# Optimization experiments

Measured on AMD Instinct MI355X. Metric: run time of the kernel, lower is better.

Reference implementation:

```python
import jax, jax.numpy as jnp
import numpy as np

B, A, C, H, S, NR = 128, 2048, 128, 512, 3, 2
PR = C + 3 + S   # 134 read params per head
PW = 3 * C + 3 + S  # 390 write params


def setup_inputs() -> dict:
    key = jax.random.key(0)
    ks = jax.random.split(key, 8)
    h = jax.random.normal(ks[0], (B, H), jnp.float32)
    mem = jax.random.normal(ks[1], (B, A, C), jnp.float32)
    ra = jax.random.uniform(ks[2], (NR, B, A), jnp.float32)
    ra = ra / ra.sum(-1, keepdims=True)  # valid attention distributions
    wa = jax.random.uniform(ks[3], (B, A), jnp.float32)
    wa = wa / wa.sum(-1, keepdims=True)
    W_read = 0.02 * jax.random.normal(ks[4], (NR, PR, H), jnp.float32)
    b_read = jnp.zeros((NR, PR), jnp.float32)
    W_write = 0.02 * jax.random.normal(ks[5], (PW, H), jnp.float32)
    b_write = jnp.zeros((PW,), jnp.float32)
    return dict(h=h, mem=mem, prev_read_attn=ra, prev_write_attn=wa,
                W_read=W_read, b_read=b_read, W_write=W_write, b_write=b_write)


def _addressing(query, beta, gate, shift, gamma, mem, prev_w):
    """NTM addressing. query [...,C] (raw), beta/gate/gamma [...,1], shift [...,S],
    mem [B,A,C] (broadcasts), prev_w [...,A]. Returns attention [...,A]."""
    eps = 1e-8
    q = jax.nn.sigmoid(query)
    beta = jax.nn.softplus(beta) + 1.0
    gate = jax.nn.sigmoid(gate)
    shift_w = jax.nn.softmax(shift, axis=-1)
    gamma = jax.nn.softplus(gamma) + 1.0
    # content-based addressing: cosine similarity + sharpened softmax over A
    qn = jnp.maximum(jnp.linalg.norm(q, axis=-1, keepdims=True), eps)      # [...,1]
    mn = jnp.maximum(jnp.linalg.norm(mem, axis=-1), eps)                   # [B,A]
    sim = jnp.einsum('...c,...ac->...a', q, mem) / (qn * mn)
    w_c = jax.nn.softmax(beta * sim, axis=-1)
    # gated interpolation with previous attention
    w_g = gate * w_c + (1.0 - gate) * prev_w
    # circular shift convolution, offsets -(S//2)..S//2
    K = S // 2
    idx = (jnp.arange(A)[:, None] - (jnp.arange(S)[None, :] - K)) % A      # [A,S]
    w_s = jnp.einsum('...as,...s->...a', w_g[..., idx], shift_w)
    # gamma sharpening
    w_pow = w_s ** gamma
    return w_pow / (w_pow.sum(-1, keepdims=True) + 1e-12)


def reference(h, mem, prev_read_attn, prev_write_attn, W_read, b_read, W_write, b_write):
    # --- read heads (vectorized over NR heads) ---
    pr = jnp.einsum('bh,rph->rbp', h, W_read) + b_read[:, None, :]         # [NR,B,PR]
    q, beta, gate, shift, gamma = jnp.split(pr, [C, C + 1, C + 2, C + 2 + S], axis=-1)
    read_w = _addressing(q, beta, gate, shift, gamma, mem, prev_read_attn)  # [NR,B,A]
    read_vectors = jnp.einsum('rba,bac->rbc', read_w, mem)                 # [NR,B,C]
    # --- write head ---
    pw = h @ W_write.T + b_write                                           # [B,PW]
    locs = np.cumsum([C, 1, 1, S, 1, C])
    qw, bw, gw, sw, gmw, erase, add = jnp.split(pw, locs.tolist(), axis=-1)
    write_w = _addressing(qw, bw, gw, sw, gmw, mem, prev_write_attn)       # [B,A]
    e = jax.nn.sigmoid(erase)[:, None, :]                                  # [B,1,C]
    a = jax.nn.sigmoid(add)[:, None, :]                                    # [B,1,C]
    w = write_w[..., None]                                                 # [B,A,1]
    new_mem = mem * (1.0 - w * e) + w * a
    return read_vectors, new_mem
```

## Files before the change

kernel.cpp:

```cpp
#include <hip/hip_runtime.h>
#include <math.h>

constexpr int B_  = 128;
constexpr int A_  = 2048;
constexpr int C_  = 128;
constexpr int H_  = 512;
constexpr int S_  = 3;
constexpr int NR_ = 2;
constexpr int PR_ = C_ + 3 + S_;
constexpr int PW_ = 3 * C_ + 3 + S_;

typedef float vfloat4 __attribute__((ext_vector_type(4)));

__device__ __forceinline__ float sigmoidf_(float x) { return 1.0f / (1.0f + expf(-x)); }
__device__ __forceinline__ float softplusf_(float x) {
  return fmaxf(x, 0.0f) + log1pf(expf(-fabsf(x)));
}

__device__ __forceinline__ float waveReduceSum(float v) {
#pragma unroll
  for (int off = 32; off; off >>= 1) v += __shfl_xor(v, off, 64);
  return v;
}
__device__ __forceinline__ float waveReduceMax(float v) {
#pragma unroll
  for (int off = 32; off; off >>= 1) v = fmaxf(v, __shfl_xor(v, off, 64));
  return v;
}

__global__ __launch_bounds__(256) void proj_kernel(
    const float* __restrict__ h, const float* __restrict__ Wr,
    const float* __restrict__ br, const float* __restrict__ Ww,
    const float* __restrict__ bw, float* __restrict__ pr, float* __restrict__ pw,
    float* __restrict__ rv) {
  constexpr int NPR = NR_ * B_ * PR_;
  constexpr int NPW = B_ * PW_;
  int gid = blockIdx.x * 256 + threadIdx.x;
  if (gid < NR_ * B_ * C_) rv[gid] = 0.0f;
  int wave = gid >> 6;
  int lane = threadIdx.x & 63;
  int out0 = wave * 2;
  const float* w0row;
  const float* w1row;
  const float* hrow;
  float bias0, bias1;
  float* outp;
  if (out0 < NPR) {
    int r = out0 / (B_ * PR_);
    int rem = out0 - r * (B_ * PR_);
    int b = rem / PR_;
    int p = rem - b * PR_;
    w0row = Wr + (size_t)(r * PR_ + p) * H_;
    w1row = w0row + H_;
    hrow = h + (size_t)b * H_;
    bias0 = br[r * PR_ + p];
    bias1 = br[r * PR_ + p + 1];
    outp = pr + out0;
  } else {
    int w2 = out0 - NPR;
    if (w2 >= NPW) return;
    int b = w2 / PW_;
    int p = w2 - b * PW_;
    w0row = Ww + (size_t)p * H_;
    w1row = w0row + H_;
    hrow = h + (size_t)b * H_;
    bias0 = bw[p];
    bias1 = bw[p + 1];
    outp = pw + w2;
  }
  const float4* h4 = (const float4*)hrow;
  const float4* wa4 = (const float4*)w0row;
  const float4* wb4 = (const float4*)w1row;
  float4 a0 = h4[(lane << 1)];
  float4 a1 = h4[(lane << 1) + 1];
  float4 b0 = wa4[(lane << 1)];
  float4 b1 = wa4[(lane << 1) + 1];
  float4 c0 = wb4[(lane << 1)];
  float4 c1 = wb4[(lane << 1) + 1];
  float acc0 = a0.x * b0.x;
  acc0 = fmaf(a0.y, b0.y, acc0);
  acc0 = fmaf(a0.z, b0.z, acc0);
  acc0 = fmaf(a0.w, b0.w, acc0);
  acc0 = fmaf(a1.x, b1.x, acc0);
  acc0 = fmaf(a1.y, b1.y, acc0);
  acc0 = fmaf(a1.z, b1.z, acc0);
  acc0 = fmaf(a1.w, b1.w, acc0);
  float acc1 = a0.x * c0.x;
  acc1 = fmaf(a0.y, c0.y, acc1);
  acc1 = fmaf(a0.z, c0.z, acc1);
  acc1 = fmaf(a0.w, c0.w, acc1);
  acc1 = fmaf(a1.x, c1.x, acc1);
  acc1 = fmaf(a1.y, c1.y, acc1);
  acc1 = fmaf(a1.z, c1.z, acc1);
  acc1 = fmaf(a1.w, c1.w, acc1);
  acc0 = waveReduceSum(acc0);
  acc1 = waveReduceSum(acc1);
  if (lane == 0) {
    outp[0] = acc0 + bias0;
    outp[1] = acc1 + bias1;
  }
}

__global__ __launch_bounds__(256) void sim_kernel(
    const float* __restrict__ mem, const float* __restrict__ pr,
    const float* __restrict__ pw, float* __restrict__ sim) {
  __shared__ __align__(16) float qs[3 * C_];
  __shared__ float iqn[3];
  int b = blockIdx.x >> 5;
  int chunk = blockIdx.x & 31;
  int rowbase = chunk << 6;
  int tid = threadIdx.x;
  for (int idx = tid; idx < 3 * C_; idx += 256) {
    int hd = idx >> 7;
    int c = idx & (C_ - 1);
    float raw = (hd < 2) ? pr[(size_t)(hd * B_ + b) * PR_ + c]
                         : pw[(size_t)b * PW_ + c];
    qs[idx] = sigmoidf_(raw);
  }
  __syncthreads();
  int wv = tid >> 6;
  int lane = tid & 63;
  if (wv < 3) {
    float v0 = qs[wv * C_ + lane];
    float v1 = qs[wv * C_ + 64 + lane];
    float ss = v0 * v0 + v1 * v1;
    ss = waveReduceSum(ss);
    if (lane == 0) iqn[wv] = 1.0f / fmaxf(sqrtf(ss), 1e-8f);
  }
  __syncthreads();

  int j = lane & 7;
  int rsub = lane >> 3;

  float4 q0[4], q1[4], q2[4];
  const float4* qs4 = (const float4*)qs;
#pragma unroll
  for (int k = 0; k < 4; k++) {
    q0[k] = qs4[j + 8 * k];
    q1[k] = qs4[32 + j + 8 * k];
    q2[k] = qs4[64 + j + 8 * k];
  }
  float iqn0 = iqn[0], iqn1 = iqn[1], iqn2 = iqn[2];

#pragma unroll
  for (int it = 0; it < 2; it++) {
    int row = rowbase + (it << 5) + (wv << 3) + rsub;
    const float4* mrow = (const float4*)(mem + ((size_t)b * A_ + row) * C_);
    float d0 = 0.f, d1 = 0.f, d2 = 0.f, ss = 0.f;
#pragma unroll
    for (int k = 0; k < 4; k++) {
      float4 m = mrow[j + 8 * k];
      d0 = fmaf(m.x, q0[k].x, d0); d0 = fmaf(m.y, q0[k].y, d0);
      d0 = fmaf(m.z, q0[k].z, d0); d0 = fmaf(m.w, q0[k].w, d0);
      d1 = fmaf(m.x, q1[k].x, d1); d1 = fmaf(m.y, q1[k].y, d1);
      d1 = fmaf(m.z, q1[k].z, d1); d1 = fmaf(m.w, q1[k].w, d1);
      d2 = fmaf(m.x, q2[k].x, d2); d2 = fmaf(m.y, q2[k].y, d2);
      d2 = fmaf(m.z, q2[k].z, d2); d2 = fmaf(m.w, q2[k].w, d2);
      ss = fmaf(m.x, m.x, ss); ss = fmaf(m.y, m.y, ss);
      ss = fmaf(m.z, m.z, ss); ss = fmaf(m.w, m.w, ss);
    }
#pragma unroll
    for (int off = 1; off <= 4; off <<= 1) {
      d0 += __shfl_xor(d0, off, 64);
      d1 += __shfl_xor(d1, off, 64);
      d2 += __shfl_xor(d2, off, 64);
      ss += __shfl_xor(ss, off, 64);
    }
    if (j == 0) {
      float imn = 1.0f / fmaxf(sqrtf(ss), 1e-8f);
      sim[(size_t)(0 * B_ + b) * A_ + row] = d0 * iqn0 * imn;
      sim[(size_t)(1 * B_ + b) * A_ + row] = d1 * iqn1 * imn;
      sim[(size_t)(2 * B_ + b) * A_ + row] = d2 * iqn2 * imn;
    }
  }
}

__global__ __launch_bounds__(1024) void attn_kernel(
    const float* __restrict__ sim, const float* __restrict__ ra,
    const float* __restrict__ wa, const float* __restrict__ pr,
    const float* __restrict__ pw, float* __restrict__ attn) {
  __shared__ float wg[A_];
  __shared__ float rb1[16], rb2[16], rb3[16];
  int hb = blockIdx.x;
  int hd = hb >> 7;
  int b = hb & (B_ - 1);
  int tid = threadIdx.x;
  int wv = tid >> 6;
  int lane = tid & 63;
  const float* src = (hd < 2) ? (pr + (size_t)hb * PR_) : (pw + (size_t)b * PW_);
  float braw = src[C_];
  float graw = src[C_ + 1];
  float s0r = src[C_ + 2], s1r = src[C_ + 3], s2r = src[C_ + 4];
  float gmraw = src[C_ + 5];
  float mx3 = fmaxf(s0r, fmaxf(s1r, s2r));
  float e0 = expf(s0r - mx3), e1 = expf(s1r - mx3), e2 = expf(s2r - mx3);
  float sinv = 1.0f / (e0 + e1 + e2);
  float beta = softplusf_(braw) + 1.0f;
  float gate = sigmoidf_(graw);
  float sw0 = e0 * sinv, sw1 = e1 * sinv, sw2 = e2 * sinv;
  float gamma = softplusf_(gmraw) + 1.0f;

  const float* simrow = sim + (size_t)hb * A_;
  const float* prev = (hd < 2) ? (ra + (size_t)hb * A_) : (wa + (size_t)b * A_);
  float* outrow = attn + (size_t)hb * A_;

  int a0 = tid;
  int a1 = tid + 1024;
  float s0 = simrow[a0];
  float s1 = simrow[a1];
  float pv0 = prev[a0];
  float pv1 = prev[a1];

  float mx = fmaxf(s0, s1);
  mx = waveReduceMax(mx);
  if (lane == 0) rb1[wv] = mx;
  __syncthreads();
  float M = rb1[0];
#pragma unroll
  for (int i = 1; i < 16; i++) M = fmaxf(M, rb1[i]);

  float p0 = expf(beta * (s0 - M));
  float p1 = expf(beta * (s1 - M));
  float l = p0 + p1;
  l = waveReduceSum(l);
  if (lane == 0) rb2[wv] = l;
  __syncthreads();
  float T = rb2[0];
#pragma unroll
  for (int i = 1; i < 16; i++) T += rb2[i];
  float inv = 1.0f / T;

  wg[a0] = fmaf(gate, p0 * inv, (1.0f - gate) * pv0);
  wg[a1] = fmaf(gate, p1 * inv, (1.0f - gate) * pv1);
  __syncthreads();

  float ws0 = sw0 * wg[(a0 + 1) & (A_ - 1)] + sw1 * wg[a0] + sw2 * wg[(a0 - 1) & (A_ - 1)];
  float ws1 = sw0 * wg[(a1 + 1) & (A_ - 1)] + sw1 * wg[a1] + sw2 * wg[(a1 - 1) & (A_ - 1)];
  float wp0 = (ws0 > 0.0f) ? exp2f(gamma * log2f(ws0)) : 0.0f;
  float wp1 = (ws1 > 0.0f) ? exp2f(gamma * log2f(ws1)) : 0.0f;
  float l2 = wp0 + wp1;
  l2 = waveReduceSum(l2);
  if (lane == 0) rb3[wv] = l2;
  __syncthreads();
  float T2 = rb3[0];
#pragma unroll
  for (int i = 1; i < 16; i++) T2 += rb3[i];
  float inv2 = 1.0f / (T2 + 1e-12f);

  outrow[a0] = wp0 * inv2;
  outrow[a1] = wp1 * inv2;
}

__global__ __launch_bounds__(256) void update_kernel(
    const float* __restrict__ mem, const float* __restrict__ attn,
    const float* __restrict__ pw, float* __restrict__ rv,
    float* __restrict__ nmem) {
  __shared__ float att0[256], att1[256], attw[256];
  __shared__ float4 red0[128];
  __shared__ float4 red1[128];
  int b = blockIdx.x >> 3;
  int chunk = blockIdx.x & 7;
  int rowbase = chunk << 8;
  int tid = threadIdx.x;
  att0[tid] = attn[(size_t)(0 * B_ + b) * A_ + rowbase + tid];
  att1[tid] = attn[(size_t)(1 * B_ + b) * A_ + rowbase + tid];
  attw[tid] = attn[(size_t)(2 * B_ + b) * A_ + rowbase + tid];
  __syncthreads();

  int rowlane = tid & 31;
  int rowoff = tid >> 5;
  int c0 = rowlane << 2;
  const float* pwrow = pw + (size_t)b * PW_;
  float2 eA = *(const float2*)(pwrow + C_ + 6 + c0);
  float2 eB = *(const float2*)(pwrow + C_ + 6 + c0 + 2);
  float2 aA = *(const float2*)(pwrow + 2 * C_ + 6 + c0);
  float2 aB = *(const float2*)(pwrow + 2 * C_ + 6 + c0 + 2);
  float e0 = sigmoidf_(eA.x), e1 = sigmoidf_(eA.y), e2 = sigmoidf_(eB.x), e3 = sigmoidf_(eB.y);
  float ad0 = sigmoidf_(aA.x), ad1 = sigmoidf_(aA.y), ad2 = sigmoidf_(aB.x), ad3 = sigmoidf_(aB.y);

  float4 acc0 = make_float4(0.f, 0.f, 0.f, 0.f);
  float4 acc1 = make_float4(0.f, 0.f, 0.f, 0.f);

#pragma unroll 4
  for (int i = 0; i < 32; i++) {
    int ridx = (i << 3) + rowoff;
    int row = rowbase + ridx;
    size_t base = ((size_t)b * A_ + row) * C_ + c0;
    float4 m = *(const float4*)(mem + base);
    float w0 = att0[ridx];
    float w1 = att1[ridx];
    float ww = attw[ridx];
    acc0.x = fmaf(w0, m.x, acc0.x);
    acc0.y = fmaf(w0, m.y, acc0.y);
    acc0.z = fmaf(w0, m.z, acc0.z);
    acc0.w = fmaf(w0, m.w, acc0.w);
    acc1.x = fmaf(w1, m.x, acc1.x);
    acc1.y = fmaf(w1, m.y, acc1.y);
    acc1.z = fmaf(w1, m.z, acc1.z);
    acc1.w = fmaf(w1, m.w, acc1.w);
    vfloat4 nm;
    nm.x = fmaf(m.x, 1.0f - ww * e0, ww * ad0);
    nm.y = fmaf(m.y, 1.0f - ww * e1, ww * ad1);
    nm.z = fmaf(m.z, 1.0f - ww * e2, ww * ad2);
    nm.w = fmaf(m.w, 1.0f - ww * e3, ww * ad3);
    __builtin_nontemporal_store(nm, (vfloat4*)(nmem + base));
  }

  int lane = tid & 63;
  int wv = tid >> 6;
  acc0.x += __shfl_xor(acc0.x, 32, 64);
  acc0.y += __shfl_xor(acc0.y, 32, 64);
  acc0.z += __shfl_xor(acc0.z, 32, 64);
  acc0.w += __shfl_xor(acc0.w, 32, 64);
  acc1.x += __shfl_xor(acc1.x, 32, 64);
  acc1.y += __shfl_xor(acc1.y, 32, 64);
  acc1.z += __shfl_xor(acc1.z, 32, 64);
  acc1.w += __shfl_xor(acc1.w, 32, 64);
  if (lane < 32) {
    red0[wv * 32 + lane] = acc0;
    red1[wv * 32 + lane] = acc1;
  }
  __syncthreads();
  if (tid < 32) {
    float4 r0 = red0[tid];
    float4 t;
    t = red0[tid + 32]; r0.x += t.x; r0.y += t.y; r0.z += t.z; r0.w += t.w;
    t = red0[tid + 64]; r0.x += t.x; r0.y += t.y; r0.z += t.z; r0.w += t.w;
    t = red0[tid + 96]; r0.x += t.x; r0.y += t.y; r0.z += t.z; r0.w += t.w;
    float4 r1 = red1[tid];
    t = red1[tid + 32]; r1.x += t.x; r1.y += t.y; r1.z += t.z; r1.w += t.w;
    t = red1[tid + 64]; r1.x += t.x; r1.y += t.y; r1.z += t.z; r1.w += t.w;
    t = red1[tid + 96]; r1.x += t.x; r1.y += t.y; r1.z += t.z; r1.w += t.w;
    float* rv0 = rv + (size_t)(0 * B_ + b) * C_ + (tid << 2);
    float* rv1 = rv + (size_t)(1 * B_ + b) * C_ + (tid << 2);
    atomicAdd(rv0 + 0, r0.x);
    atomicAdd(rv0 + 1, r0.y);
    atomicAdd(rv0 + 2, r0.z);
    atomicAdd(rv0 + 3, r0.w);
    atomicAdd(rv1 + 0, r1.x);
    atomicAdd(rv1 + 1, r1.y);
    atomicAdd(rv1 + 2, r1.z);
    atomicAdd(rv1 + 3, r1.w);
  }
}

extern "C" void kernel_launch(void* const* d_in, const int* in_sizes, int n_in,
                              void* d_out, int out_size, void* d_ws, size_t ws_size,
                              hipStream_t stream) {
  const float* h   = (const float*)d_in[0];
  const float* mem = (const float*)d_in[1];
  const float* ra  = (const float*)d_in[2];
  const float* wa  = (const float*)d_in[3];
  const float* Wr  = (const float*)d_in[4];
  const float* br  = (const float*)d_in[5];
  const float* Ww  = (const float*)d_in[6];
  const float* bw  = (const float*)d_in[7];

  float* out = (float*)d_out;
  float* rv = out;
  float* nmem = out + NR_ * B_ * C_;

  float* ws = (float*)d_ws;
  float* pr_buf = ws;
  float* pw_buf = pr_buf + NR_ * B_ * PR_;
  float* simb   = pw_buf + B_ * PW_;

  constexpr int NPAIRS = (NR_ * B_ * PR_ + B_ * PW_) / 2;
  proj_kernel<<<dim3(NPAIRS / 4), dim3(256), 0, stream>>>(h, Wr, br, Ww, bw, pr_buf, pw_buf, rv);
  sim_kernel<<<dim3(B_ * (A_ / 64)), dim3(256), 0, stream>>>(mem, pr_buf, pw_buf, simb);
  attn_kernel<<<dim3(3 * B_), dim3(1024), 0, stream>>>(simb, ra, wa, pr_buf, pw_buf, simb);
  update_kernel<<<dim3(B_ * (A_ / 256)), dim3(256), 0, stream>>>(mem, simb, pw_buf, rv, nmem);
}
```

Measured before the change: 289.1 us.

## Fuse similarity, addressing and memory update into one per-batch kernel

The separate sim, attention and update kernels are merged into a single kernel with one 1024-thread block per batch element. Similarities and attention weights now stay in shared memory instead of round-tripping through a workspace buffer. The read vectors are reduced in-block and stored directly, which removes the atomics and the zero-init of the output in the projection kernel. The cost is that the grid shrinks to 128 blocks, which may leave many compute units idle. Each block also streams its 1 MB memory slice twice, relying on cache for the second pass.

```diff
diff --git a/kernel.cpp b/kernel.cpp
--- a/kernel.cpp
+++ b/kernel.cpp
@@ -31,13 +31,10 @@
 __global__ __launch_bounds__(256) void proj_kernel(
     const float* __restrict__ h, const float* __restrict__ Wr,
     const float* __restrict__ br, const float* __restrict__ Ww,
-    const float* __restrict__ bw, float* __restrict__ pr, float* __restrict__ pw,
-    float* __restrict__ rv) {
+    const float* __restrict__ bw, float* __restrict__ pr, float* __restrict__ pw) {
   constexpr int NPR = NR_ * B_ * PR_;
   constexpr int NPW = B_ * PW_;
-  int gid = blockIdx.x * 256 + threadIdx.x;
-  if (gid < NR_ * B_ * C_) rv[gid] = 0.0f;
-  int wave = gid >> 6;
+  int wave = (blockIdx.x * blockDim.x + threadIdx.x) >> 6;
   int lane = threadIdx.x & 63;
   int out0 = wave * 2;
   const float* w0row;
@@ -101,25 +98,31 @@
   }
 }
 
-__global__ __launch_bounds__(256) void sim_kernel(
-    const float* __restrict__ mem, const float* __restrict__ pr,
-    const float* __restrict__ pw, float* __restrict__ sim) {
+__global__ __launch_bounds__(1024) void mega_kernel(
+    const float* __restrict__ mem, const float* __restrict__ ra,
+    const float* __restrict__ wa, const float* __restrict__ pr,
+    const float* __restrict__ pw, float* __restrict__ rv,
+    float* __restrict__ nmem) {
+  __shared__ float sims[3][A_];
+  __shared__ float wg[A_];
   __shared__ __align__(16) float qs[3 * C_];
   __shared__ float iqn[3];
-  int b = blockIdx.x >> 5;
-  int chunk = blockIdx.x & 31;
-  int rowbase = chunk << 6;
+  __shared__ float rbuf[16];
+  __shared__ float4 red[2][16][32];
+
+  int b = blockIdx.x;
   int tid = threadIdx.x;
-  for (int idx = tid; idx < 3 * C_; idx += 256) {
-    int hd = idx >> 7;
-    int c = idx & (C_ - 1);
+  int lane = tid & 63;
+  int wv = tid >> 6;
+
+  if (tid < 3 * C_) {
+    int hd = tid >> 7;
+    int c = tid & (C_ - 1);
     float raw = (hd < 2) ? pr[(size_t)(hd * B_ + b) * PR_ + c]
                          : pw[(size_t)b * PW_ + c];
-    qs[idx] = sigmoidf_(raw);
+    qs[tid] = sigmoidf_(raw);
   }
   __syncthreads();
-  int wv = tid >> 6;
-  int lane = tid & 63;
   if (wv < 3) {
     float v0 = qs[wv * C_ + lane];
     float v1 = qs[wv * C_ + 64 + lane];
@@ -129,218 +132,185 @@
   }
   __syncthreads();
 
-  int j = lane & 7;
-  int rsub = lane >> 3;
-
-  float4 q0[4], q1[4], q2[4];
-  const float4* qs4 = (const float4*)qs;
-#pragma unroll
-  for (int k = 0; k < 4; k++) {
-    q0[k] = qs4[j + 8 * k];
-    q1[k] = qs4[32 + j + 8 * k];
-    q2[k] = qs4[64 + j + 8 * k];
-  }
-  float iqn0 = iqn[0], iqn1 = iqn[1], iqn2 = iqn[2];
-
-#pragma unroll
-  for (int it = 0; it < 2; it++) {
-    int row = rowbase + (it << 5) + (wv << 3) + rsub;
-    const float4* mrow = (const float4*)(mem + ((size_t)b * A_ + row) * C_);
-    float d0 = 0.f, d1 = 0.f, d2 = 0.f, ss = 0.f;
+  {
+    int j = tid & 7;
+    int rgrp = tid >> 3;
+    float4 q0[4], q1[4], q2[4];
+    const float4* qs4 = (const float4*)qs;
 #pragma unroll
     for (int k = 0; k < 4; k++) {
-      float4 m = mrow[j + 8 * k];
-      d0 = fmaf(m.x, q0[k].x, d0); d0 = fmaf(m.y, q0[k].y, d0);
-      d0 = fmaf(m.z, q0[k].z, d0); d0 = fmaf(m.w, q0[k].w, d0);
-      d1 = fmaf(m.x, q1[k].x, d1); d1 = fmaf(m.y, q1[k].y, d1);
-      d1 = fmaf(m.z, q1[k].z, d1); d1 = fmaf(m.w, q1[k].w, d1);
-      d2 = fmaf(m.x, q2[k].x, d2); d2 = fmaf(m.y, q2[k].y, d2);
-      d2 = fmaf(m.z, q2[k].z, d2); d2 = fmaf(m.w, q2[k].w, d2);
-      ss = fmaf(m.x, m.x, ss); ss = fmaf(m.y, m.y, ss);
-      ss = fmaf(m.z, m.z, ss); ss = fmaf(m.w, m.w, ss);
-    }
-#pragma unroll
-    for (int off = 1; off <= 4; off <<= 1) {
-      d0 += __shfl_xor(d0, off, 64);
-      d1 += __shfl_xor(d1, off, 64);
-      d2 += __shfl_xor(d2, off, 64);
-      ss += __shfl_xor(ss, off, 64);
-    }
-    if (j == 0) {
-      float imn = 1.0f / fmaxf(sqrtf(ss), 1e-8f);
-      sim[(size_t)(0 * B_ + b) * A_ + row] = d0 * iqn0 * imn;
-      sim[(size_t)(1 * B_ + b) * A_ + row] = d1 * iqn1 * imn;
-      sim[(size_t)(2 * B_ + b) * A_ + row] = d2 * iqn2 * imn;
-    }
-  }
-}
-
-__global__ __launch_bounds__(1024) void attn_kernel(
-    const float* __restrict__ sim, const float* __restrict__ ra,
-    const float* __restrict__ wa, const float* __restrict__ pr,
-    const float* __restrict__ pw, float* __restrict__ attn) {
-  __shared__ float wg[A_];
-  __shared__ float rb1[16], rb2[16], rb3[16];
-  int hb = blockIdx.x;
-  int hd = hb >> 7;
-  int b = hb & (B_ - 1);
-  int tid = threadIdx.x;
-  int wv = tid >> 6;
-  int lane = tid & 63;
-  const float* src = (hd < 2) ? (pr + (size_t)hb * PR_) : (pw + (size_t)b * PW_);
-  float braw = src[C_];
-  float graw = src[C_ + 1];
-  float s0r = src[C_ + 2], s1r = src[C_ + 3], s2r = src[C_ + 4];
-  float gmraw = src[C_ + 5];
-  float mx3 = fmaxf(s0r, fmaxf(s1r, s2r));
-  float e0 = expf(s0r - mx3), e1 = expf(s1r - mx3), e2 = expf(s2r - mx3);
-  float sinv = 1.0f / (e0 + e1 + e2);
-  float beta = softplusf_(braw) + 1.0f;
-  float gate = sigmoidf_(graw);
-  float sw0 = e0 * sinv, sw1 = e1 * sinv, sw2 = e2 * sinv;
-  float gamma = softplusf_(gmraw) + 1.0f;
-
-  const float* simrow = sim + (size_t)hb * A_;
-  const float* prev = (hd < 2) ? (ra + (size_t)hb * A_) : (wa + (size_t)b * A_);
-  float* outrow = attn + (size_t)hb * A_;
-
-  int a0 = tid;
-  int a1 = tid + 1024;
-  float s0 = simrow[a0];
-  float s1 = simrow[a1];
-  float pv0 = prev[a0];
-  float pv1 = prev[a1];
-
-  float mx = fmaxf(s0, s1);
-  mx = waveReduceMax(mx);
-  if (lane == 0) rb1[wv] = mx;
+      q0[k] = qs4[j + 8 * k];
+      q1[k] = qs4[32 + j + 8 * k];
+      q2[k] = qs4[64 + j + 8 * k];
+    }
+    float iq0 = iqn[0], iq1 = iqn[1], iq2 = iqn[2];
+#pragma unroll 2
+    for (int i = 0; i < 16; i++) {
+      int row = (i << 7) + rgrp;
+      const float4* mrow = (const float4*)(mem + ((size_t)b * A_ + row) * C_);
+      float d0 = 0.f, d1 = 0.f, d2 = 0.f, ss = 0.f;
+#pragma unroll
+      for (int k = 0; k < 4; k++) {
+        float4 m = mrow[j + 8 * k];
+        d0 = fmaf(m.x, q0[k].x, d0); d0 = fmaf(m.y, q0[k].y, d0);
+        d0 = fmaf(m.z, q0[k].z, d0); d0 = fmaf(m.w, q0[k].w, d0);
+        d1 = fmaf(m.x, q1[k].x, d1); d1 = fmaf(m.y, q1[k].y, d1);
+        d1 = fmaf(m.z, q1[k].z, d1); d1 = fmaf(m.w, q1[k].w, d1);
+        d2 = fmaf(m.x, q2[k].x, d2); d2 = fmaf(m.y, q2[k].y, d2);
+        d2 = fmaf(m.z, q2[k].z, d2); d2 = fmaf(m.w, q2[k].w, d2);
+        ss = fmaf(m.x, m.x, ss); ss = fmaf(m.y, m.y, ss);
+        ss = fmaf(m.z, m.z, ss); ss = fmaf(m.w, m.w, ss);
+      }
+#pragma unroll
+      for (int off = 1; off <= 4; off <<= 1) {
+        d0 += __shfl_xor(d0, off, 64);
+        d1 += __shfl_xor(d1, off, 64);
+        d2 += __shfl_xor(d2, off, 64);
+        ss += __shfl_xor(ss, off, 64);
+      }
+      if (j == 0) {
+        float imn = 1.0f / fmaxf(sqrtf(ss), 1e-8f);
+        sims[0][row] = d0 * iq0 * imn;
+        sims[1][row] = d1 * iq1 * imn;
+        sims[2][row] = d2 * iq2 * imn;
+      }
+    }
+  }
   __syncthreads();
-  float M = rb1[0];
-#pragma unroll
-  for (int i = 1; i < 16; i++) M = fmaxf(M, rb1[i]);
-
-  float p0 = expf(beta * (s0 - M));
-  float p1 = expf(beta * (s1 - M));
-  float l = p0 + p1;
-  l = waveReduceSum(l);
-  if (lane == 0) rb2[wv] = l;
-  __syncthreads();
-  float T = rb2[0];
-#pragma unroll
-  for (int i = 1; i < 16; i++) T += rb2[i];
-  float inv = 1.0f / T;
-
-  wg[a0] = fmaf(gate, p0 * inv, (1.0f - gate) * pv0);
-  wg[a1] = fmaf(gate, p1 * inv, (1.0f - gate) * pv1);
-  __syncthreads();
-
-  float ws0 = sw0 * wg[(a0 + 1) & (A_ - 1)] + sw1 * wg[a0] + sw2 * wg[(a0 - 1) & (A_ - 1)];
-  float ws1 = sw0 * wg[(a1 + 1) & (A_ - 1)] + sw1 * wg[a1] + sw2 * wg[(a1 - 1) & (A_ - 1)];
-  float wp0 = (ws0 > 0.0f) ? exp2f(gamma * log2f(ws0)) : 0.0f;
-  float wp1 = (ws1 > 0.0f) ? exp2f(gamma * log2f(ws1)) : 0.0f;
-  float l2 = wp0 + wp1;
-  l2 = waveReduceSum(l2);
-  if (lane == 0) rb3[wv] = l2;
-  __syncthreads();
-  float T2 = rb3[0];
-#pragma unroll
-  for (int i = 1; i < 16; i++) T2 += rb3[i];
-  float inv2 = 1.0f / (T2 + 1e-12f);
-
-  outrow[a0] = wp0 * inv2;
-  outrow[a1] = wp1 * inv2;
-}
-
-__global__ __launch_bounds__(256) void update_kernel(
-    const float* __restrict__ mem, const float* __restrict__ attn,
-    const float* __restrict__ pw, float* __restrict__ rv,
-    float* __restrict__ nmem) {
-  __shared__ float att0[256], att1[256], attw[256];
-  __shared__ float4 red0[128];
-  __shared__ float4 red1[128];
-  int b = blockIdx.x >> 3;
-  int chunk = blockIdx.x & 7;
-  int rowbase = chunk << 8;
-  int tid = threadIdx.x;
-  att0[tid] = attn[(size_t)(0 * B_ + b) * A_ + rowbase + tid];
-  att1[tid] = attn[(size_t)(1 * B_ + b) * A_ + rowbase + tid];
-  attw[tid] = attn[(size_t)(2 * B_ + b) * A_ + rowbase + tid];
-  __syncthreads();
-
-  int rowlane = tid & 31;
-  int rowoff = tid >> 5;
-  int c0 = rowlane << 2;
-  const float* pwrow = pw + (size_t)b * PW_;
-  float2 eA = *(const float2*)(pwrow + C_ + 6 + c0);
-  float2 eB = *(const float2*)(pwrow + C_ + 6 + c0 + 2);
-  float2 aA = *(const float2*)(pwrow + 2 * C_ + 6 + c0);
-  float2 aB = *(const float2*)(pwrow + 2 * C_ + 6 + c0 + 2);
-  float e0 = sigmoidf_(eA.x), e1 = sigmoidf_(eA.y), e2 = sigmoidf_(eB.x), e3 = sigmoidf_(eB.y);
-  float ad0 = sigmoidf_(aA.x), ad1 = sigmoidf_(aA.y), ad2 = sigmoidf_(aB.x), ad3 = sigmoidf_(aB.y);
-
-  float4 acc0 = make_float4(0.f, 0.f, 0.f, 0.f);
-  float4 acc1 = make_float4(0.f, 0.f, 0.f, 0.f);
+
+  for (int hd = 0; hd < 3; hd++) {
+    const float* src = (hd < 2) ? (pr + (size_t)(hd * B_ + b) * PR_)
+                                : (pw + (size_t)b * PW_);
+    float braw = src[C_];
+    float graw = src[C_ + 1];
+    float s0r = src[C_ + 2], s1r = src[C_ + 3], s2r = src[C_ + 4];
+    float gmraw = src[C_ + 5];
+    float mx3 = fmaxf(s0r, fmaxf(s1r, s2r));
+    float e0 = expf(s0r - mx3), e1 = expf(s1r - mx3), e2 = expf(s2r - mx3);
+    float sinv = 1.0f / (e0 + e1 + e2);
+    float beta = softplusf_(braw) + 1.0f;
+    float gate = sigmoidf_(graw);
+    float sw0 = e0 * sinv, sw1 = e1 * sinv, sw2 = e2 * sinv;
+    float gamma = softplusf_(gmraw) + 1.0f;
+    const float* prev = (hd < 2) ? (ra + (size_t)(hd * B_ + b) * A_)
+                                 : (wa + (size_t)b * A_);
+
+    float s0 = sims[hd][tid];
+    float s1 = sims[hd][tid + 1024];
+    float pv0 = prev[tid];
+    float pv1 = prev[tid + 1024];
+
+    float mx = fmaxf(s0, s1);
+    mx = waveReduceMax(mx);
+    if (lane == 0) rbuf[wv] = mx;
+    __syncthreads();
+    float M = rbuf[0];
+#pragma unroll
+    for (int i = 1; i < 16; i++) M = fmaxf(M, rbuf[i]);
+    __syncthreads();
+
+    float p0 = expf(beta * (s0 - M));
+    float p1 = expf(beta * (s1 - M));
+    float l = p0 + p1;
+    l = waveReduceSum(l);
+    if (lane == 0) rbuf[wv] = l;
+    __syncthreads();
+    float T = rbuf[0];
+#pragma unroll
+    for (int i = 1; i < 16; i++) T += rbuf[i];
+    float inv = 1.0f / T;
+
+    wg[tid] = fmaf(gate, p0 * inv, (1.0f - gate) * pv0);
+    wg[tid + 1024] = fmaf(gate, p1 * inv, (1.0f - gate) * pv1);
+    __syncthreads();
+
+    float ws0 = sw0 * wg[(tid + 1) & (A_ - 1)] + sw1 * wg[tid] +
+                sw2 * wg[(tid - 1) & (A_ - 1)];
+    float ws1 = sw0 * wg[(tid + 1025) & (A_ - 1)] + sw1 * wg[tid + 1024] +
+                sw2 * wg[(tid + 1023) & (A_ - 1)];
+    float wp0 = (ws0 > 0.0f) ? exp2f(gamma * log2f(ws0)) : 0.0f;
+    float wp1 = (ws1 > 0.0f) ? exp2f(gamma * log2f(ws1)) : 0.0f;
+    float l2 = wp0 + wp1;
+    l2 = waveReduceSum(l2);
+    __syncthreads();
+    if (lane == 0) rbuf[wv] = l2;
+    __syncthreads();
+    float T2 = rbuf[0];
+#pragma unroll
+    for (int i = 1; i < 16; i++) T2 += rbuf[i];
+    float inv2 = 1.0f / (T2 + 1e-12f);
+    sims[hd][tid] = wp0 * inv2;
+    sims[hd][tid + 1024] = wp1 * inv2;
+    __syncthreads();
+  }
+
+  {
+    int quad = tid & 31;
+    int rgrp = tid >> 5;
+    int c0 = quad << 2;
+    const float* pwrow = pw + (size_t)b * PW_;
+    float2 eA = *(const float2*)(pwrow + C_ + 6 + c0);
+    float2 eB = *(const float2*)(pwrow + C_ + 6 + c0 + 2);
+    float2 aA = *(const float2*)(pwrow + 2 * C_ + 6 + c0);
+    float2 aB = *(const float2*)(pwrow + 2 * C_ + 6 + c0 + 2);
+    float e0 = sigmoidf_(eA.x), e1 = sigmoidf_(eA.y), e2 = sigmoidf_(eB.x), e3 = sigmoidf_(eB.y);
+    float ad0 = sigmoidf_(aA.x), ad1 = sigmoidf_(aA.y), ad2 = sigmoidf_(aB.x), ad3 = sigmoidf_(aB.y);
+
+    float4 acc0 = make_float4(0.f, 0.f, 0.f, 0.f);
+    float4 acc1 = make_float4(0.f, 0.f, 0.f, 0.f);
 
 #pragma unroll 4
-  for (int i = 0; i < 32; i++) {
-    int ridx = (i << 3) + rowoff;
-    int row = rowbase + ridx;
-    size_t base = ((size_t)b * A_ + row) * C_ + c0;
-    float4 m = *(const float4*)(mem + base);
-    float w0 = att0[ridx];
-    float w1 = att1[ridx];
-    float ww = attw[ridx];
-    acc0.x = fmaf(w0, m.x, acc0.x);
-    acc0.y = fmaf(w0, m.y, acc0.y);
-    acc0.z = fmaf(w0, m.z, acc0.z);
-    acc0.w = fmaf(w0, m.w, acc0.w);
-    acc1.x = fmaf(w1, m.x, acc1.x);
-    acc1.y = fmaf(w1, m.y, acc1.y);
-    acc1.z = fmaf(w1, m.z, acc1.z);
-    acc1.w = fmaf(w1, m.w, acc1.w);
-    vfloat4 nm;
-    nm.x = fmaf(m.x, 1.0f - ww * e0, ww * ad0);
-    nm.y = fmaf(m.y, 1.0f - ww * e1, ww * ad1);
-    nm.z = fmaf(m.z, 1.0f - ww * e2, ww * ad2);
-    nm.w = fmaf(m.w, 1.0f - ww * e3, ww * ad3);
-    __builtin_nontemporal_store(nm, (vfloat4*)(nmem + base));
-  }
-
-  int lane = tid & 63;
-  int wv = tid >> 6;
-  acc0.x += __shfl_xor(acc0.x, 32, 64);
-  acc0.y += __shfl_xor(acc0.y, 32, 64);
-  acc0.z += __shfl_xor(acc0.z, 32, 64);
-  acc0.w += __shfl_xor(acc0.w, 32, 64);
-  acc1.x += __shfl_xor(acc1.x, 32, 64);
-  acc1.y += __shfl_xor(acc1.y, 32, 64);
-  acc1.z += __shfl_xor(acc1.z, 32, 64);
-  acc1.w += __shfl_xor(acc1.w, 32, 64);
-  if (lane < 32) {
-    red0[wv * 32 + lane] = acc0;
-    red1[wv * 32 + lane] = acc1;
-  }
-  __syncthreads();
-  if (tid < 32) {
-    float4 r0 = red0[tid];
-    float4 t;
-    t = red0[tid + 32]; r0.x += t.x; r0.y += t.y; r0.z += t.z; r0.w += t.w;
-    t = red0[tid + 64]; r0.x += t.x; r0.y += t.y; r0.z += t.z; r0.w += t.w;
-    t = red0[tid + 96]; r0.x += t.x; r0.y += t.y; r0.z += t.z; r0.w += t.w;
-    float4 r1 = red1[tid];
-    t = red1[tid + 32]; r1.x += t.x; r1.y += t.y; r1.z += t.z; r1.w += t.w;
-    t = red1[tid + 64]; r1.x += t.x; r1.y += t.y; r1.z += t.z; r1.w += t.w;
-    t = red1[tid + 96]; r1.x += t.x; r1.y += t.y; r1.z += t.z; r1.w += t.w;
-    float* rv0 = rv + (size_t)(0 * B_ + b) * C_ + (tid << 2);
-    float* rv1 = rv + (size_t)(1 * B_ + b) * C_ + (tid << 2);
-    atomicAdd(rv0 + 0, r0.x);
-    atomicAdd(rv0 + 1, r0.y);
-    atomicAdd(rv0 + 2, r0.z);
-    atomicAdd(rv0 + 3, r0.w);
-    atomicAdd(rv1 + 0, r1.x);
-    atomicAdd(rv1 + 1, r1.y);
-    atomicAdd(rv1 + 2, r1.z);
-    atomicAdd(rv1 + 3, r1.w);
+    for (int i = 0; i < 64; i++) {
+      int row = (i << 5) + rgrp;
+      size_t base = ((size_t)b * A_ + row) * C_ + c0;
+      float4 m = *(const float4*)(mem + base);
+      float w0 = sims[0][row];
+      float w1 = sims[1][row];
+      float ww = sims[2][row];
+      acc0.x = fmaf(w0, m.x, acc0.x);
+      acc0.y = fmaf(w0, m.y, acc0.y);
+      acc0.z = fmaf(w0, m.z, acc0.z);
+      acc0.w = fmaf(w0, m.w, acc0.w);
+      acc1.x = fmaf(w1, m.x, acc1.x);
+      acc1.y = fmaf(w1, m.y, acc1.y);
+      acc1.z = fmaf(w1, m.z, acc1.z);
+      acc1.w = fmaf(w1, m.w, acc1.w);
+      vfloat4 nm;
+      nm.x = fmaf(m.x, 1.0f - ww * e0, ww * ad0);
+      nm.y = fmaf(m.y, 1.0f - ww * e1, ww * ad1);
+      nm.z = fmaf(m.z, 1.0f - ww * e2, ww * ad2);
+      nm.w = fmaf(m.w, 1.0f - ww * e3, ww * ad3);
+      __builtin_nontemporal_store(nm, (vfloat4*)(nmem + base));
+    }
+
+    acc0.x += __shfl_xor(acc0.x, 32, 64);
+    acc0.y += __shfl_xor(acc0.y, 32, 64);
+    acc0.z += __shfl_xor(acc0.z, 32, 64);
+    acc0.w += __shfl_xor(acc0.w, 32, 64);
+    acc1.x += __shfl_xor(acc1.x, 32, 64);
+    acc1.y += __shfl_xor(acc1.y, 32, 64);
+    acc1.z += __shfl_xor(acc1.z, 32, 64);
+    acc1.w += __shfl_xor(acc1.w, 32, 64);
+    if (lane < 32) {
+      red[0][wv][lane] = acc0;
+      red[1][wv][lane] = acc1;
+    }
+    __syncthreads();
+    if (tid < 64) {
+      int hd = tid >> 5;
+      int q = tid & 31;
+      float4 r = red[hd][0][q];
+#pragma unroll
+      for (int g = 1; g < 16; g++) {
+        float4 t = red[hd][g][q];
+        r.x += t.x; r.y += t.y; r.z += t.z; r.w += t.w;
+      }
+      float* rvp = rv + (size_t)(hd * B_ + b) * C_ + (q << 2);
+      rvp[0] = r.x;
+      rvp[1] = r.y;
+      rvp[2] = r.z;
+      rvp[3] = r.w;
+    }
   }
 }
 
@@ -363,11 +333,8 @@
   float* ws = (float*)d_ws;
   float* pr_buf = ws;
   float* pw_buf = pr_buf + NR_ * B_ * PR_;
-  float* simb   = pw_buf + B_ * PW_;
 
   constexpr int NPAIRS = (NR_ * B_ * PR_ + B_ * PW_) / 2;
-  proj_kernel<<<dim3(NPAIRS / 4), dim3(256), 0, stream>>>(h, Wr, br, Ww, bw, pr_buf, pw_buf, rv);
-  sim_kernel<<<dim3(B_ * (A_ / 64)), dim3(256), 0, stream>>>(mem, pr_buf, pw_buf, simb);
-  attn_kernel<<<dim3(3 * B_), dim3(1024), 0, stream>>>(simb, ra, wa, pr_buf, pw_buf, simb);
-  update_kernel<<<dim3(B_ * (A_ / 256)), dim3(256), 0, stream>>>(mem, simb, pw_buf, rv, nmem);
-}
+  proj_kernel<<<dim3(NPAIRS / 4), dim3(256), 0, stream>>>(h, Wr, br, Ww, bw, pr_buf, pw_buf);
+  mega_kernel<<<dim3(B_), dim3(1024), 0, stream>>>(mem, ra, wa, pr_buf, pw_buf, rv, nmem);
+}
```

After: 293.0 us. Within noise of the previous version (+1.4%).
